# Performance work log

Hardware: AMD Instinct MI355X
Metric: run time of the kernel (lower is better)

Reference implementation:

```python
import jax, jax.numpy as jnp
import numpy as np

EMBED_DIM = 64
NUM_EXPERTS = 4
SELECT_TOP_K = 2
N_TOKENS = 2097152


def setup_inputs() -> dict:
    key = jax.random.key(0)
    kx, kw = jax.random.split(key)
    x = jax.random.normal(kx, (N_TOKENS, EMBED_DIM), dtype=jnp.float32)
    # nn.Linear(64, 4, bias=False) weight: [out_features, in_features]
    W = jax.random.normal(kw, (NUM_EXPERTS, EMBED_DIM), dtype=jnp.float32) * (1.0 / np.sqrt(EMBED_DIM))
    return {"x": x, "W": W}


def reference(x, W):
    # logits: [N, E] = x @ W.T (Linear without bias)
    logits = jnp.einsum('nd,ed->ne', x, W)
    # top-k over experts
    topk_logits, topk_indices = jax.lax.top_k(logits, SELECT_TOP_K)  # [N, K]
    topk_probs = jax.nn.softmax(topk_logits, axis=-1)                # [N, K]
    # scatter top-k probs into dense [N, E] routing-weight tensor
    rows = jnp.arange(logits.shape[0])[:, None]                      # [N, 1]
    weights = jnp.zeros_like(logits).at[rows, topk_indices].set(topk_probs)
    return weights, topk_indices
```

## Files before the change

### kernel.cpp

```cpp
#include <hip/hip_runtime.h>
#include <math.h>

#define EMBED_DIM 64
#define NUM_EXPERTS 4
#define THREADS 128
#define TOKS_PER_WAVE 32
#define TILE_CHUNKS 512
#define NBLOCKS 32768

__global__ __launch_bounds__(THREADS) void gate_kernel(
    const float* __restrict__ x,
    const float* __restrict__ W,
    float* __restrict__ wout,
    float* __restrict__ iout,
    int n)
{
#pragma clang fp contract(off)
    __shared__ float4 lds[2 * TILE_CHUNKS];

    const int lane = threadIdx.x & 63;
    const int wid  = threadIdx.x >> 6;
    const int tile = blockIdx.x * 2 + wid;
    float4* tilebuf = &lds[wid * TILE_CHUNKS];

    const float4* x4 = reinterpret_cast<const float4*>(x);
    const float4* W4 = reinterpret_cast<const float4*>(W);

    const size_t tileChunk = (size_t)tile * TILE_CHUNKS;
    float4 r[8];
    #pragma unroll
    for (int i = 0; i < 8; ++i) {
        r[i] = x4[tileChunk + i * 64 + lane];
    }

    #pragma unroll
    for (int i = 0; i < 8; ++i) {
        const int G  = i * 64 + lane;
        const int tk = G >> 4;
        const int c  = G & 15;
        tilebuf[(tk << 4) | (c ^ (tk & 7))] = r[i];
    }
    __builtin_amdgcn_sched_barrier(0);

    if (lane < TOKS_PER_WAVE) {
        float s0 = 0.0f, s1 = 0.0f, s2 = 0.0f, s3 = 0.0f;
        #pragma unroll
        for (int j = 0; j < 16; ++j) {
            const float4 xv = tilebuf[(lane << 4) | (j ^ (lane & 7))];
            const float4 a = W4[ 0 + j];
            const float4 b = W4[16 + j];
            const float4 c = W4[32 + j];
            const float4 d = W4[48 + j];
            s0 = s0 + xv.x * a.x; s0 = s0 + xv.y * a.y;
            s0 = s0 + xv.z * a.z; s0 = s0 + xv.w * a.w;
            s1 = s1 + xv.x * b.x; s1 = s1 + xv.y * b.y;
            s1 = s1 + xv.z * b.z; s1 = s1 + xv.w * b.w;
            s2 = s2 + xv.x * c.x; s2 = s2 + xv.y * c.y;
            s2 = s2 + xv.z * c.z; s2 = s2 + xv.w * c.w;
            s3 = s3 + xv.x * d.x; s3 = s3 + xv.y * d.y;
            s3 = s3 + xv.z * d.z; s3 = s3 + xv.w * d.w;
        }

        int   i1 = 0;  float v1 = s0;
        if (s1 > v1) { v1 = s1; i1 = 1; }
        if (s2 > v1) { v1 = s2; i1 = 2; }
        if (s3 > v1) { v1 = s3; i1 = 3; }
        int   i2 = -1; float v2 = -INFINITY;
        if (i1 != 0 && s0 > v2) { v2 = s0; i2 = 0; }
        if (i1 != 1 && s1 > v2) { v2 = s1; i2 = 1; }
        if (i1 != 2 && s2 > v2) { v2 = s2; i2 = 2; }
        if (i1 != 3 && s3 > v2) { v2 = s3; i2 = 3; }

        const float e2  = expf(v2 - v1);
        const float den = 1.0f + e2;
        const float p1  = 1.0f / den;
        const float p2  = e2 / den;

        const int tok = tile * TOKS_PER_WAVE + lane;

        float4 wv;
        wv.x = (i1 == 0) ? p1 : ((i2 == 0) ? p2 : 0.0f);
        wv.y = (i1 == 1) ? p1 : ((i2 == 1) ? p2 : 0.0f);
        wv.z = (i1 == 2) ? p1 : ((i2 == 2) ? p2 : 0.0f);
        wv.w = (i1 == 3) ? p1 : ((i2 == 3) ? p2 : 0.0f);
        reinterpret_cast<float4*>(wout)[tok] = wv;

        float2 iv;
        iv.x = (float)i1;
        iv.y = (float)i2;
        reinterpret_cast<float2*>(iout)[tok] = iv;
    }
}

extern "C" void kernel_launch(void* const* d_in, const int* in_sizes, int n_in,
                              void* d_out, int out_size, void* d_ws, size_t ws_size,
                              hipStream_t stream) {
    const float* x = (const float*)d_in[0];
    const float* W = (const float*)d_in[1];
    const int n = in_sizes[0] / EMBED_DIM;

    float* wout = (float*)d_out;
    float* iout = wout + (size_t)n * NUM_EXPERTS;

    hipLaunchKernelGGL(gate_kernel, dim3(NBLOCKS), dim3(THREADS), 0, stream,
                       x, W, wout, iout, n);
}
```

Measured before the change: 115.0 us.

## Use persistent waves with register double-buffered tile prefetch

Replaces the one-tile-per-wave grid of 32768 blocks with a persistent grid of 1280 blocks. Each wave strides over tiles and loads the next tile into registers while it transposes and processes the current one through LDS. The goal is to hide global load latency behind compute and cut block launch overhead. The cost is higher register pressure from two 8-float4 buffers and fewer resident waves to hide latency through occupancy.

```diff
diff --git a/kernel.cpp b/kernel.cpp
--- a/kernel.cpp
+++ b/kernel.cpp
@@ -4,9 +4,9 @@
 #define EMBED_DIM 64
 #define NUM_EXPERTS 4
 #define THREADS 128
-#define TOKS_PER_WAVE 32
-#define TILE_CHUNKS 512
-#define NBLOCKS 32768
+#define TOKS 32
+#define CH 512
+#define NBLOCKS 1280
 
 __global__ __launch_bounds__(THREADS) void gate_kernel(
     const float* __restrict__ x,
@@ -16,79 +16,107 @@
     int n)
 {
 #pragma clang fp contract(off)
-    __shared__ float4 lds[2 * TILE_CHUNKS];
+    __shared__ float4 lds[2 * 2 * CH];
 
     const int lane = threadIdx.x & 63;
     const int wid  = threadIdx.x >> 6;
-    const int tile = blockIdx.x * 2 + wid;
-    float4* tilebuf = &lds[wid * TILE_CHUNKS];
+    const int gw   = blockIdx.x * 2 + wid;
+    const int NW   = NBLOCKS * 2;
+    const int ntiles = n / TOKS;
 
     const float4* x4 = reinterpret_cast<const float4*>(x);
     const float4* W4 = reinterpret_cast<const float4*>(W);
+    float4* buf0 = &lds[(wid * 2 + 0) * CH];
+    float4* buf1 = &lds[(wid * 2 + 1) * CH];
 
-    const size_t tileChunk = (size_t)tile * TILE_CHUNKS;
-    float4 r[8];
-    #pragma unroll
-    for (int i = 0; i < 8; ++i) {
-        r[i] = x4[tileChunk + i * 64 + lane];
-    }
+    float4 rA[8], rB[8];
 
-    #pragma unroll
-    for (int i = 0; i < 8; ++i) {
-        const int G  = i * 64 + lane;
-        const int tk = G >> 4;
-        const int c  = G & 15;
-        tilebuf[(tk << 4) | (c ^ (tk & 7))] = r[i];
-    }
-    __builtin_amdgcn_sched_barrier(0);
+    auto LOAD = [&](float4 (&r)[8], int tile) {
+        const size_t tc = (size_t)tile * CH;
+        #pragma unroll
+        for (int i = 0; i < 8; ++i) r[i] = x4[tc + i * 64 + lane];
+    };
 
-    if (lane < TOKS_PER_WAVE) {
-        float s0 = 0.0f, s1 = 0.0f, s2 = 0.0f, s3 = 0.0f;
+    auto PROCESS = [&](const float4 (&r)[8], int tile, float4* buf) {
         #pragma unroll
-        for (int j = 0; j < 16; ++j) {
-            const float4 xv = tilebuf[(lane << 4) | (j ^ (lane & 7))];
-            const float4 a = W4[ 0 + j];
-            const float4 b = W4[16 + j];
-            const float4 c = W4[32 + j];
-            const float4 d = W4[48 + j];
-            s0 = s0 + xv.x * a.x; s0 = s0 + xv.y * a.y;
-            s0 = s0 + xv.z * a.z; s0 = s0 + xv.w * a.w;
-            s1 = s1 + xv.x * b.x; s1 = s1 + xv.y * b.y;
-            s1 = s1 + xv.z * b.z; s1 = s1 + xv.w * b.w;
-            s2 = s2 + xv.x * c.x; s2 = s2 + xv.y * c.y;
-            s2 = s2 + xv.z * c.z; s2 = s2 + xv.w * c.w;
-            s3 = s3 + xv.x * d.x; s3 = s3 + xv.y * d.y;
-            s3 = s3 + xv.z * d.z; s3 = s3 + xv.w * d.w;
+        for (int i = 0; i < 8; ++i) {
+            const int G  = i * 64 + lane;
+            const int tk = G >> 4;
+            const int c  = G & 15;
+            buf[(tk << 4) | (c ^ (tk & 7))] = r[i];
         }
+        if (lane < TOKS) {
+            float s0 = 0.0f, s1 = 0.0f, s2 = 0.0f, s3 = 0.0f;
+            #pragma unroll
+            for (int j = 0; j < 16; ++j) {
+                const float4 xv = buf[(lane << 4) | (j ^ (lane & 7))];
+                const float4 a = W4[ 0 + j];
+                const float4 b = W4[16 + j];
+                const float4 c = W4[32 + j];
+                const float4 d = W4[48 + j];
+                s0 = s0 + xv.x * a.x; s0 = s0 + xv.y * a.y;
+                s0 = s0 + xv.z * a.z; s0 = s0 + xv.w * a.w;
+                s1 = s1 + xv.x * b.x; s1 = s1 + xv.y * b.y;
+                s1 = s1 + xv.z * b.z; s1 = s1 + xv.w * b.w;
+                s2 = s2 + xv.x * c.x; s2 = s2 + xv.y * c.y;
+                s2 = s2 + xv.z * c.z; s2 = s2 + xv.w * c.w;
+                s3 = s3 + xv.x * d.x; s3 = s3 + xv.y * d.y;
+                s3 = s3 + xv.z * d.z; s3 = s3 + xv.w * d.w;
+            }
+            int   i1 = 0;  float v1 = s0;
+            if (s1 > v1) { v1 = s1; i1 = 1; }
+            if (s2 > v1) { v1 = s2; i1 = 2; }
+            if (s3 > v1) { v1 = s3; i1 = 3; }
+            int   i2 = -1; float v2 = -INFINITY;
+            if (i1 != 0 && s0 > v2) { v2 = s0; i2 = 0; }
+            if (i1 != 1 && s1 > v2) { v2 = s1; i2 = 1; }
+            if (i1 != 2 && s2 > v2) { v2 = s2; i2 = 2; }
+            if (i1 != 3 && s3 > v2) { v2 = s3; i2 = 3; }
 
-        int   i1 = 0;  float v1 = s0;
-        if (s1 > v1) { v1 = s1; i1 = 1; }
-        if (s2 > v1) { v1 = s2; i1 = 2; }
-        if (s3 > v1) { v1 = s3; i1 = 3; }
-        int   i2 = -1; float v2 = -INFINITY;
-        if (i1 != 0 && s0 > v2) { v2 = s0; i2 = 0; }
-        if (i1 != 1 && s1 > v2) { v2 = s1; i2 = 1; }
-        if (i1 != 2 && s2 > v2) { v2 = s2; i2 = 2; }
-        if (i1 != 3 && s3 > v2) { v2 = s3; i2 = 3; }
+            const float e2  = expf(v2 - v1);
+            const float den = 1.0f + e2;
+            const float p1  = 1.0f / den;
+            const float p2  = e2 / den;
 
-        const float e2  = expf(v2 - v1);
-        const float den = 1.0f + e2;
-        const float p1  = 1.0f / den;
-        const float p2  = e2 / den;
+            const int tok = tile * TOKS + lane;
+            float4 wv;
+            wv.x = (i1 == 0) ? p1 : ((i2 == 0) ? p2 : 0.0f);
+            wv.y = (i1 == 1) ? p1 : ((i2 == 1) ? p2 : 0.0f);
+            wv.z = (i1 == 2) ? p1 : ((i2 == 2) ? p2 : 0.0f);
+            wv.w = (i1 == 3) ? p1 : ((i2 == 3) ? p2 : 0.0f);
+            reinterpret_cast<float4*>(wout)[tok] = wv;
+            float2 iv;
+            iv.x = (float)i1;
+            iv.y = (float)i2;
+            reinterpret_cast<float2*>(iout)[tok] = iv;
+        }
+    };
 
-        const int tok = tile * TOKS_PER_WAVE + lane;
+    int tA = gw;
+    if (tA >= ntiles) return;
+    LOAD(rA, tA);
 
-        float4 wv;
-        wv.x = (i1 == 0) ? p1 : ((i2 == 0) ? p2 : 0.0f);
-        wv.y = (i1 == 1) ? p1 : ((i2 == 1) ? p2 : 0.0f);
-        wv.z = (i1 == 2) ? p1 : ((i2 == 2) ? p2 : 0.0f);
-        wv.w = (i1 == 3) ? p1 : ((i2 == 3) ? p2 : 0.0f);
-        reinterpret_cast<float4*>(wout)[tok] = wv;
-
-        float2 iv;
-        iv.x = (float)i1;
-        iv.y = (float)i2;
-        reinterpret_cast<float2*>(iout)[tok] = iv;
+    for (;;) {
+        const int tB = tA + NW;
+        if (tB < ntiles) {
+            LOAD(rB, tB);
+            __builtin_amdgcn_sched_barrier(0);
+            PROCESS(rA, tA, buf0);
+            const int tA2 = tB + NW;
+            if (tA2 < ntiles) {
+                LOAD(rA, tA2);
+                __builtin_amdgcn_sched_barrier(0);
+                PROCESS(rB, tB, buf1);
+                tA = tA2;
+                continue;
+            } else {
+                PROCESS(rB, tB, buf1);
+                break;
+            }
+        } else {
+            PROCESS(rA, tA, buf0);
+            break;
+        }
     }
 }
 
```

Result: slower. 259.3 us (+125.4%).
